# Optimization experiments

Measured on AMD Instinct MI355X. Metric: run time of the kernel, lower is better.

Reference implementation:

```python
import jax, jax.numpy as jnp
import numpy as np
from jax import lax

NUM_CLASSES = 4   # includes ignore label 0
IGNORE = 0
MAX_SAMPLES = 1024
HALF = MAX_SAMPLES // 2
BIG = 1 << 30     # sentinel key for invalid/unselected pixels


def setup_inputs() -> dict:
    key = jax.random.key(0)
    k1, k2, k3 = jax.random.split(key, 3)
    B, C, H, W = 4, 64, 256, 256
    feat_map = jax.random.normal(k1, (B, C, H, W), dtype=jnp.float32)
    labels = jax.random.randint(k2, (B, H, W), 0, NUM_CLASSES, dtype=jnp.int32)
    preds = jax.random.normal(k3, (B, NUM_CLASSES, H, W), dtype=jnp.float32)
    return {"feat_map": feat_map, "labels": labels, "preds": preds}


def _soft_dilate2d(x):
    # F.max_pool2d(x, kernel=3, stride=1, padding=1) on [B,1,H,W]
    return lax.reduce_window(x, -jnp.inf, lax.max, (1, 1, 3, 3), (1, 1, 1, 1), "SAME")


def _per_pair(fm, lab, pd, cls):
    # fm: [C, N] features, lab: [N] int labels, pd: [N] dilated pred class, cls: scalar int
    N = lab.shape[0]
    ar = jnp.arange(N)
    clsf = cls.astype(pd.dtype)
    in_cls = lab == cls
    hard = (pd != clsf) & in_cls   # mispredicted (after dilation) pixels of this class
    easy = (pd == clsf) & in_cls
    # torch code uses randperm; reference uses the deterministic identity
    # permutation: keep the first HALF hard pixels (in raster order).
    hard_key = jnp.where(hard, ar, BIG)
    hard_top = jnp.sort(hard_key)[:HALF]                      # [HALF]
    valid_h = (hard_top < BIG).astype(fm.dtype)
    feat_h = fm[:, jnp.where(hard_top < BIG, hard_top, 0)] * valid_h  # [C, HALF], zero-padded
    # rest pool = leftover hard pixels (rank >= HALF) first, then easy pixels;
    # keep first HALF of that concatenation.
    hard_rank = jnp.cumsum(hard) - 1
    easy_rank = jnp.cumsum(easy) - 1
    excess = jnp.maximum(jnp.sum(hard) - HALF, 0)
    rest_key = jnp.where(hard & (hard_rank >= HALF), hard_rank - HALF,
                         jnp.where(easy, excess + easy_rank, BIG))
    order = jnp.argsort(rest_key)[:HALF]                      # pixel indices, valid first
    valid_r = (jnp.take(rest_key, order) < BIG).astype(fm.dtype)
    feat_r = fm[:, order] * valid_r                           # [C, HALF], zero-padded
    return jnp.concatenate([feat_h, feat_r], axis=1)          # [C, MAX_SAMPLES]


def reference(feat_map, labels, preds):
    B, C, H, W = feat_map.shape
    N = H * W
    # softmax preserves argmax -> skip the softmax
    pred_lab = jnp.argmax(preds, axis=1).astype(feat_map.dtype)[:, None]  # [B,1,H,W]
    preds_d = _soft_dilate2d(pred_lab).reshape(B, N)
    feat_flat = feat_map.reshape(B, C, N)
    lab_flat = labels.reshape(B, N)
    # assume all non-ignore classes present in each image (true w.h.p. for
    # random labels over 65536 pixels) -> static total_classes = B*(NUM_CLASSES-1)
    b_idx = jnp.repeat(jnp.arange(B), NUM_CLASSES - 1)
    cls_idx = jnp.tile(jnp.arange(1, NUM_CLASSES), B)
    feat_extract = jax.vmap(_per_pair)(feat_flat[b_idx], lab_flat[b_idx],
                                       preds_d[b_idx], cls_idx)  # [B*(NC-1), C, 1024]
    feat_label = cls_idx.astype(jnp.float32)
    return feat_extract, feat_label
```

## Files before the change

### kernel.cpp

```cpp
#include <hip/hip_runtime.h>

#define BB 4
#define CC 64
#define HH 256
#define WW 256
#define NPIX (HH*WW)
#define NCLS 4
#define NPAIR 12
#define HALF 512
#define MAXS 1024
#define NOUT (NPAIR*CC*MAXS)
#define CHUNK 4096
#define NCHUNK (NPIX/CHUNK)
#define NBAND 64
#define BANDPIX (NPIX/NBAND)


__global__ void __launch_bounds__(256) k_dargmax(
        const float* __restrict__ preds, const int* __restrict__ labels,
        unsigned char* __restrict__ pd, unsigned* __restrict__ bandCounts) {
    __shared__ unsigned char vm[4][WW];
    __shared__ unsigned wsum[4][3];
    int bx = blockIdx.x;
    int b = bx >> 6, band = bx & 63;
    int y0 = band * 4;
    int x = threadIdx.x;
    const float* pb = preds + (size_t)b * NCLS * NPIX;

    unsigned char am[6];
#pragma unroll
    for (int r = 0; r < 6; ++r) {
        int y = y0 + r - 1;
        unsigned char a = 0;
        if (y >= 0 && y < HH) {
            const float* p = pb + y * WW + x;
            float best = p[0];
            int arg = 0;
#pragma unroll
            for (int c = 1; c < NCLS; ++c) {
                float v = p[(size_t)c * NPIX];
                if (v > best) { best = v; arg = c; }
            }
            a = (unsigned char)arg;
        }
        am[r] = a;
    }
    unsigned char vmr[4];
#pragma unroll
    for (int ry = 0; ry < 4; ++ry) {
        int m = am[ry];
        if (am[ry + 1] > m) m = am[ry + 1];
        if (am[ry + 2] > m) m = am[ry + 2];
        vmr[ry] = (unsigned char)m;
        vm[ry][x] = (unsigned char)m;
    }
    __syncthreads();

    unsigned pk[3] = {0u, 0u, 0u};
#pragma unroll
    for (int ry = 0; ry < 4; ++ry) {
        int m = vmr[ry];
        if (x > 0)      { int v = vm[ry][x - 1]; if (v > m) m = v; }
        if (x < WW - 1) { int v = vm[ry][x + 1]; if (v > m) m = v; }
        int idx = b * NPIX + (y0 + ry) * WW + x;
        pd[idx] = (unsigned char)m;
        int l = labels[idx];
#pragma unroll
        for (int c = 0; c < 3; ++c)
            if (l == c + 1) pk[c] += (m == c + 1) ? (1u << 16) : 1u;
    }
    int lane = x & 63, w = x >> 6;
#pragma unroll
    for (int c = 0; c < 3; ++c)
#pragma unroll
        for (int off = 32; off > 0; off >>= 1)
            pk[c] += (unsigned)__shfl_down((int)pk[c], off, 64);
    if (lane == 0) { wsum[w][0] = pk[0]; wsum[w][1] = pk[1]; wsum[w][2] = pk[2]; }
    __syncthreads();
    if (x < 3)
        bandCounts[(b * 3 + x) * NBAND + band] =
            wsum[0][x] + wsum[1][x] + wsum[2][x] + wsum[3][x];
}

__global__ void __launch_bounds__(256) k_assign(
        const int* __restrict__ labels, const unsigned char* __restrict__ pd,
        const unsigned* __restrict__ bandCounts, unsigned* __restrict__ pairTotals,
        int* __restrict__ slots, float* __restrict__ out) {
    int pair = blockIdx.x >> 4, chunk = blockIdx.x & 15;
    int b = pair / 3, cls = pair % 3 + 1;
    int t = threadIdx.x;
    __shared__ unsigned bc[NBAND];
    __shared__ unsigned ws[4];
    if (t < NBAND) bc[t] = bandCounts[pair * NBAND + t];
    __syncthreads();
    unsigned base = 0, total = 0;
    int cut = chunk * 4;
#pragma unroll
    for (int i = 0; i < NBAND; ++i) {
        unsigned v = bc[i];
        total += v;
        if (i < cut) base += v;
    }
    if (chunk == 0 && t == 0) {
        pairTotals[pair] = total;
        out[NOUT + pair] = (float)cls;
    }
    int excess = (int)(total & 0xffffu) - HALF;
    if (excess < 0) excess = 0;
    int baseH = (int)(base & 0xffffu), baseE = (int)(base >> 16);
    if (baseH >= MAXS && HALF + excess + baseE >= MAXS) return;

    const int4* lab4 = (const int4*)(labels + b * NPIX + chunk * CHUNK + t * 16);
    const uint4* pd16 = (const uint4*)(pd + b * NPIX + chunk * CHUNK + t * 16);
    int4 l0 = lab4[0], l1 = lab4[1], l2 = lab4[2], l3 = lab4[3];
    uint4 dp = pd16[0];
    int ls[16] = {l0.x, l0.y, l0.z, l0.w, l1.x, l1.y, l1.z, l1.w,
                  l2.x, l2.y, l2.z, l2.w, l3.x, l3.y, l3.z, l3.w};
    unsigned char ds[16];
    unsigned dw[4] = {dp.x, dp.y, dp.z, dp.w};
#pragma unroll
    for (int j = 0; j < 16; ++j) ds[j] = (dw[j >> 2] >> ((j & 3) * 8)) & 0xff;

    unsigned mine = 0;
#pragma unroll
    for (int j = 0; j < 16; ++j)
        if (ls[j] == cls) mine += (ds[j] == cls) ? (1u << 16) : 1u;

    int lane = t & 63, w = t >> 6;
    unsigned v = mine;
#pragma unroll
    for (int off = 1; off < 64; off <<= 1) {
        unsigned u = (unsigned)__shfl_up((int)v, off, 64);
        if (lane >= off) v += u;
    }
    if (lane == 63) ws[w] = v;
    __syncthreads();
    unsigned waveBase = 0;
    for (int i = 0; i < w; ++i) waveBase += ws[i];
    unsigned excl = waveBase + v - mine;

    int hr = baseH + (int)(excl & 0xffffu);
    int er = baseE + (int)(excl >> 16);
    int pixBase = chunk * CHUNK + t * 16;
    int* sl = slots + pair * MAXS;
#pragma unroll
    for (int j = 0; j < 16; ++j) {
        if (ls[j] == cls) {
            if (ds[j] != cls) {
                if (hr < MAXS) sl[hr] = pixBase + j;
                hr++;
            } else {
                int pos = HALF + excess + er;
                if (pos < MAXS) sl[pos] = pixBase + j;
                er++;
            }
        }
    }
}

__global__ void __launch_bounds__(256) k_gather(
        const float* __restrict__ feat, const int* __restrict__ slots,
        const unsigned* __restrict__ pairTotals, float* __restrict__ out) {
    int i = blockIdx.x * 256 + threadIdx.x;
    int q = i << 2;
    int pair = q >> 16;
    unsigned tot = pairTotals[pair];
    int Nh = (int)(tot & 0xffffu), Ne = (int)(tot >> 16);
    int excess = Nh - HALF; if (excess < 0) excess = 0;
    int hardEnd = Nh < MAXS ? Nh : MAXS;
    int easyStart = HALF + excess;
    int easyEnd = easyStart + Ne; if (easyEnd > MAXS) easyEnd = MAXS;

    int c = (q >> 10) & (CC - 1);
    int slot = q & (MAXS - 1);
    int b = pair / 3;
    const float* fp = feat + ((size_t)(b * CC + c)) * NPIX;
    const int* sp = slots + pair * MAXS + slot;
    float o[4];
#pragma unroll
    for (int j = 0; j < 4; ++j) {
        int s = slot + j;
        bool valid = (s < hardEnd) || (s >= easyStart && s < easyEnd);
        float val = 0.0f;
        if (valid) val = fp[sp[j]];
        o[j] = val;
    }
    ((float4*)out)[i] = make_float4(o[0], o[1], o[2], o[3]);
}

extern "C" void kernel_launch(void* const* d_in, const int* in_sizes, int n_in,
                              void* d_out, int out_size, void* d_ws, size_t ws_size,
                              hipStream_t stream) {
    const float* feat   = (const float*)d_in[0];
    const int*   labels = (const int*)d_in[1];
    const float* preds  = (const float*)d_in[2];
    float* out = (float*)d_out;

    unsigned char* pd = (unsigned char*)d_ws;
    int* slots = (int*)(pd + BB * NPIX);
    unsigned* bandCounts = (unsigned*)(slots + NPAIR * MAXS);
    unsigned* pairTotals = bandCounts + NPAIR * NBAND;

    k_dargmax<<<NBAND * BB, 256, 0, stream>>>(preds, labels, pd, bandCounts);
    k_assign<<<NPAIR * NCHUNK, 256, 0, stream>>>(labels, pd, bandCounts, pairTotals, slots, out);
    k_gather<<<NOUT / 4 / 256, 256, 0, stream>>>(feat, slots, pairTotals, out);
}
```

Baseline: 105.4 us.

## Fuse assign into count kernel with per-band compaction buffers and binary-search gather

The separate assign kernel is removed. The dilated-argmax kernel now uses wave ballots and an in-block prefix to write each hard and easy pixel index into per-(pair, band) compaction buffers, and it no longer writes the pd byte map. The gather kernel rebuilds the band prefix sums in shared memory and binary-searches them to find each slot's source pixel. This saves one launch and a global round trip. The cost is that every pixel index is written, not only the first 1024, and each gather block repeats the prefix scan and the searches.

```diff
diff --git a/kernel.cpp b/kernel.cpp
--- a/kernel.cpp
+++ b/kernel.cpp
@@ -10,17 +10,17 @@
 #define HALF 512
 #define MAXS 1024
 #define NOUT (NPAIR*CC*MAXS)
-#define CHUNK 4096
-#define NCHUNK (NPIX/CHUNK)
 #define NBAND 64
 #define BANDPIX (NPIX/NBAND)
 
 
-__global__ void __launch_bounds__(256) k_dargmax(
+__global__ void __launch_bounds__(256) k_count(
         const float* __restrict__ preds, const int* __restrict__ labels,
-        unsigned char* __restrict__ pd, unsigned* __restrict__ bandCounts) {
+        int* __restrict__ hardBuf, int* __restrict__ easyBuf,
+        unsigned* __restrict__ bandCounts) {
     __shared__ unsigned char vm[4][WW];
-    __shared__ unsigned wsum[4][3];
+    __shared__ unsigned short cnt[96];
+    __shared__ unsigned short pre[96];
     int bx = blockIdx.x;
     int b = bx >> 6, band = bx & 63;
     int y0 = band * 4;
@@ -56,136 +56,116 @@
     }
     __syncthreads();
 
-    unsigned pk[3] = {0u, 0u, 0u};
+    int lane = x & 63, w = x >> 6;
+    unsigned long long lt = (1ull << lane) - 1ull;
+
+    int labv[4], pos[4], cls4[4], typ4[4];
 #pragma unroll
     for (int ry = 0; ry < 4; ++ry) {
         int m = vmr[ry];
         if (x > 0)      { int v = vm[ry][x - 1]; if (v > m) m = v; }
         if (x < WW - 1) { int v = vm[ry][x + 1]; if (v > m) m = v; }
-        int idx = b * NPIX + (y0 + ry) * WW + x;
-        pd[idx] = (unsigned char)m;
-        int l = labels[idx];
+        int l = labels[b * NPIX + (y0 + ry) * WW + x];
+        labv[ry] = l;
+        cls4[ry] = l - 1;
+        typ4[ry] = (m == l) ? 1 : 0;
+        int p = 0;
 #pragma unroll
-        for (int c = 0; c < 3; ++c)
-            if (l == c + 1) pk[c] += (m == c + 1) ? (1u << 16) : 1u;
+        for (int c = 1; c <= 3; ++c) {
+            unsigned long long hm = __ballot(l == c && m != c);
+            unsigned long long em = __ballot(l == c && m == c);
+            if (lane == 0) {
+                cnt[((c - 1) * 2 + 0) * 16 + ry * 4 + w] = (unsigned short)__popcll(hm);
+                cnt[((c - 1) * 2 + 1) * 16 + ry * 4 + w] = (unsigned short)__popcll(em);
+            }
+            if (l == c) p = (int)__popcll(((m != c) ? hm : em) & lt);
+        }
+        pos[ry] = p;
     }
-    int lane = x & 63, w = x >> 6;
+    __syncthreads();
+
+    if (x < 96) {
+        int base = x & ~15, k = x & 15;
+        int s = 0;
+        for (int j = 0; j < k; ++j) s += cnt[base + j];
+        pre[x] = (unsigned short)s;
+    }
+    __syncthreads();
+
+    if (x < 3) {
+        int th = pre[(x * 2 + 0) * 16 + 15] + cnt[(x * 2 + 0) * 16 + 15];
+        int te = pre[(x * 2 + 1) * 16 + 15] + cnt[(x * 2 + 1) * 16 + 15];
+        bandCounts[(b * 3 + x) * NBAND + band] = (unsigned)th | ((unsigned)te << 16);
+    }
 #pragma unroll
-    for (int c = 0; c < 3; ++c)
-#pragma unroll
-        for (int off = 32; off > 0; off >>= 1)
-            pk[c] += (unsigned)__shfl_down((int)pk[c], off, 64);
-    if (lane == 0) { wsum[w][0] = pk[0]; wsum[w][1] = pk[1]; wsum[w][2] = pk[2]; }
-    __syncthreads();
-    if (x < 3)
-        bandCounts[(b * 3 + x) * NBAND + band] =
-            wsum[0][x] + wsum[1][x] + wsum[2][x] + wsum[3][x];
-}
-
-__global__ void __launch_bounds__(256) k_assign(
-        const int* __restrict__ labels, const unsigned char* __restrict__ pd,
-        const unsigned* __restrict__ bandCounts, unsigned* __restrict__ pairTotals,
-        int* __restrict__ slots, float* __restrict__ out) {
-    int pair = blockIdx.x >> 4, chunk = blockIdx.x & 15;
-    int b = pair / 3, cls = pair % 3 + 1;
-    int t = threadIdx.x;
-    __shared__ unsigned bc[NBAND];
-    __shared__ unsigned ws[4];
-    if (t < NBAND) bc[t] = bandCounts[pair * NBAND + t];
-    __syncthreads();
-    unsigned base = 0, total = 0;
-    int cut = chunk * 4;
-#pragma unroll
-    for (int i = 0; i < NBAND; ++i) {
-        unsigned v = bc[i];
-        total += v;
-        if (i < cut) base += v;
-    }
-    if (chunk == 0 && t == 0) {
-        pairTotals[pair] = total;
-        out[NOUT + pair] = (float)cls;
-    }
-    int excess = (int)(total & 0xffffu) - HALF;
-    if (excess < 0) excess = 0;
-    int baseH = (int)(base & 0xffffu), baseE = (int)(base >> 16);
-    if (baseH >= MAXS && HALF + excess + baseE >= MAXS) return;
-
-    const int4* lab4 = (const int4*)(labels + b * NPIX + chunk * CHUNK + t * 16);
-    const uint4* pd16 = (const uint4*)(pd + b * NPIX + chunk * CHUNK + t * 16);
-    int4 l0 = lab4[0], l1 = lab4[1], l2 = lab4[2], l3 = lab4[3];
-    uint4 dp = pd16[0];
-    int ls[16] = {l0.x, l0.y, l0.z, l0.w, l1.x, l1.y, l1.z, l1.w,
-                  l2.x, l2.y, l2.z, l2.w, l3.x, l3.y, l3.z, l3.w};
-    unsigned char ds[16];
-    unsigned dw[4] = {dp.x, dp.y, dp.z, dp.w};
-#pragma unroll
-    for (int j = 0; j < 16; ++j) ds[j] = (dw[j >> 2] >> ((j & 3) * 8)) & 0xff;
-
-    unsigned mine = 0;
-#pragma unroll
-    for (int j = 0; j < 16; ++j)
-        if (ls[j] == cls) mine += (ds[j] == cls) ? (1u << 16) : 1u;
-
-    int lane = t & 63, w = t >> 6;
-    unsigned v = mine;
-#pragma unroll
-    for (int off = 1; off < 64; off <<= 1) {
-        unsigned u = (unsigned)__shfl_up((int)v, off, 64);
-        if (lane >= off) v += u;
-    }
-    if (lane == 63) ws[w] = v;
-    __syncthreads();
-    unsigned waveBase = 0;
-    for (int i = 0; i < w; ++i) waveBase += ws[i];
-    unsigned excl = waveBase + v - mine;
-
-    int hr = baseH + (int)(excl & 0xffffu);
-    int er = baseE + (int)(excl >> 16);
-    int pixBase = chunk * CHUNK + t * 16;
-    int* sl = slots + pair * MAXS;
-#pragma unroll
-    for (int j = 0; j < 16; ++j) {
-        if (ls[j] == cls) {
-            if (ds[j] != cls) {
-                if (hr < MAXS) sl[hr] = pixBase + j;
-                hr++;
-            } else {
-                int pos = HALF + excess + er;
-                if (pos < MAXS) sl[pos] = pixBase + j;
-                er++;
-            }
+    for (int ry = 0; ry < 4; ++ry) {
+        int cc = cls4[ry];
+        if (cc >= 0) {
+            int c2 = cc * 2 + typ4[ry];
+            int r = pre[c2 * 16 + ry * 4 + w] + pos[ry];
+            int pair = b * 3 + cc;
+            int* buf = typ4[ry] ? easyBuf : hardBuf;
+            buf[(((pair << 6) | band) << 10) + r] = (y0 + ry) * WW + x;
         }
     }
 }
 
 __global__ void __launch_bounds__(256) k_gather(
-        const float* __restrict__ feat, const int* __restrict__ slots,
-        const unsigned* __restrict__ pairTotals, float* __restrict__ out) {
-    int i = blockIdx.x * 256 + threadIdx.x;
-    int q = i << 2;
-    int pair = q >> 16;
-    unsigned tot = pairTotals[pair];
-    int Nh = (int)(tot & 0xffffu), Ne = (int)(tot >> 16);
+        const float* __restrict__ feat, const int* __restrict__ hardBuf,
+        const int* __restrict__ easyBuf, const unsigned* __restrict__ bandCounts,
+        float* __restrict__ out) {
+    __shared__ int cumH[NBAND + 1], cumE[NBAND + 1];
+    int blk = blockIdx.x;
+    int pair = blk >> 6, c = blk & 63;
+    int t = threadIdx.x;
+    if (t < NBAND) {
+        unsigned v = bandCounts[pair * NBAND + t];
+        int hv = (int)(v & 0xffffu), ev = (int)(v >> 16);
+#pragma unroll
+        for (int off = 1; off < 64; off <<= 1) {
+            int hu = __shfl_up(hv, off, 64);
+            int eu = __shfl_up(ev, off, 64);
+            if (t >= off) { hv += hu; ev += eu; }
+        }
+        cumH[t + 1] = hv;
+        cumE[t + 1] = ev;
+        if (t == 0) { cumH[0] = 0; cumE[0] = 0; }
+    }
+    __syncthreads();
+
+    int Nh = cumH[NBAND], Ne = cumE[NBAND];
     int excess = Nh - HALF; if (excess < 0) excess = 0;
     int hardEnd = Nh < MAXS ? Nh : MAXS;
     int easyStart = HALF + excess;
     int easyEnd = easyStart + Ne; if (easyEnd > MAXS) easyEnd = MAXS;
+    if (c == 0 && t == 0) out[NOUT + pair] = (float)(pair % 3 + 1);
 
-    int c = (q >> 10) & (CC - 1);
-    int slot = q & (MAXS - 1);
     int b = pair / 3;
-    const float* fp = feat + ((size_t)(b * CC + c)) * NPIX;
-    const int* sp = slots + pair * MAXS + slot;
+    const float* fp = feat + (size_t)(b * CC + c) * NPIX;
     float o[4];
 #pragma unroll
     for (int j = 0; j < 4; ++j) {
-        int s = slot + j;
-        bool valid = (s < hardEnd) || (s >= easyStart && s < easyEnd);
+        int s = t * 4 + j;
+        bool isH = s < hardEnd;
+        bool isE = (s >= easyStart) & (s < easyEnd);
         float val = 0.0f;
-        if (valid) val = fp[sp[j]];
+        if (isH | isE) {
+            int r = isH ? s : s - easyStart;
+            const int* cum = isH ? cumH : cumE;
+            int lo = 0, hi = NBAND;
+#pragma unroll
+            for (int it = 0; it < 6; ++it) {
+                int mid = (lo + hi) >> 1;
+                if (cum[mid] <= r) lo = mid; else hi = mid;
+            }
+            int off = r - cum[lo];
+            const int* buf = isH ? hardBuf : easyBuf;
+            int pix = buf[(((pair << 6) | lo) << 10) + off];
+            val = fp[pix];
+        }
         o[j] = val;
     }
-    ((float4*)out)[i] = make_float4(o[0], o[1], o[2], o[3]);
+    ((float4*)out)[blk * 256 + t] = make_float4(o[0], o[1], o[2], o[3]);
 }
 
 extern "C" void kernel_launch(void* const* d_in, const int* in_sizes, int n_in,
@@ -196,12 +176,10 @@
     const float* preds  = (const float*)d_in[2];
     float* out = (float*)d_out;
 
-    unsigned char* pd = (unsigned char*)d_ws;
-    int* slots = (int*)(pd + BB * NPIX);
-    unsigned* bandCounts = (unsigned*)(slots + NPAIR * MAXS);
-    unsigned* pairTotals = bandCounts + NPAIR * NBAND;
+    int* hardBuf = (int*)d_ws;
+    int* easyBuf = hardBuf + NPAIR * NBAND * 1024;
+    unsigned* bandCounts = (unsigned*)(easyBuf + NPAIR * NBAND * 1024);
 
-    k_dargmax<<<NBAND * BB, 256, 0, stream>>>(preds, labels, pd, bandCounts);
-    k_assign<<<NPAIR * NCHUNK, 256, 0, stream>>>(labels, pd, bandCounts, pairTotals, slots, out);
-    k_gather<<<NOUT / 4 / 256, 256, 0, stream>>>(feat, slots, pairTotals, out);
+    k_count<<<NBAND * BB, 256, 0, stream>>>(preds, labels, hardBuf, easyBuf, bandCounts);
+    k_gather<<<NPAIR * CC, 256, 0, stream>>>(feat, hardBuf, easyBuf, bandCounts, out);
 }
```

After: 103.7 us. Within noise of the previous version (-1.7%).
